# Optimization experiments

Hardware: AMD Instinct MI355X
Metric: run time of the kernel (lower is better)

Reference implementation:

```python
import jax, jax.numpy as jnp
import numpy as np
from jax import lax

N, C, RC, H, W = 2, 256, 32, 64, 64  # RC = C // 8


def conv1x1(x, w, b):
    # x: [n,c,h,w], w: [o,c], b: [o]
    return jnp.einsum('nchw,oc->nohw', x, w) + b[None, :, None, None]


def conv3x3(x, w, b):
    # x: [n,c,h,w], w: [o,i,3,3]
    y = lax.conv_general_dilated(x, w, window_strides=(1, 1), padding='SAME',
                                 dimension_numbers=('NCHW', 'OIHW', 'NCHW'))
    return y + b[None, :, None, None]


def setup_inputs() -> dict:
    key = jax.random.key(0)
    ks = jax.random.split(key, 16)
    p = lambda k, s: jax.random.normal(k, s, dtype=jnp.float32) * 0.02
    z = lambda o: jnp.zeros((o,), jnp.float32)
    return {
        'rgb_feat': jax.random.normal(ks[0], (N, C, H, W), jnp.float32),
        'chm_feat': jax.random.normal(ks[1], (N, C, H, W), jnp.float32),
        'rgb_q_w': p(ks[2], (RC, C)), 'rgb_q_b': z(RC),
        'rgb_k_w': p(ks[3], (RC, C)), 'rgb_k_b': z(RC),
        'rgb_v_w': p(ks[4], (C, C)), 'rgb_v_b': z(C),
        'depth_q_w': p(ks[5], (RC, C)), 'depth_q_b': z(RC),
        'depth_k_w': p(ks[6], (RC, C)), 'depth_k_b': z(RC),
        'depth_v_w': p(ks[7], (C, C)), 'depth_v_b': z(C),
        'gate_w': p(ks[8], (C, 2 * C)), 'gate_b': z(C),
        'fus1_w': p(ks[9], (2 * C, 2 * C)), 'fus1_b': z(2 * C),
        'fus2_w': p(ks[10], (2 * C, 2 * C, 3, 3)), 'fus2_b': z(2 * C),
        'fus3_w': p(ks[11], (C, 2 * C)), 'fus3_b': z(C),
        'skip_w': p(ks[12], (C, 2 * C)), 'skip_b': z(C),
    }


def reference(rgb_feat, chm_feat,
              rgb_q_w, rgb_q_b, rgb_k_w, rgb_k_b, rgb_v_w, rgb_v_b,
              depth_q_w, depth_q_b, depth_k_w, depth_k_b, depth_v_w, depth_v_b,
              gate_w, gate_b, fus1_w, fus1_b, fus2_w, fus2_b,
              fus3_w, fus3_b, skip_w, skip_b):
    n, c, h, w = rgb_feat.shape
    hw = h * w
    flat = lambda t: t.reshape(n, t.shape[1], hw)

    rq = flat(conv1x1(rgb_feat, rgb_q_w, rgb_q_b))       # [n,rc,hw]
    rk = flat(conv1x1(rgb_feat, rgb_k_w, rgb_k_b))       # [n,rc,hw]
    rv = flat(conv1x1(rgb_feat, rgb_v_w, rgb_v_b))       # [n,c,hw]
    dq = flat(conv1x1(chm_feat, depth_q_w, depth_q_b))   # [n,rc,hw]
    dk = flat(conv1x1(chm_feat, depth_k_w, depth_k_b))   # [n,rc,hw]
    dv = flat(conv1x1(chm_feat, depth_v_w, depth_v_b))   # [n,c,hw]

    # rgb branch attended with depth-derived attention
    rgb_attn = jax.nn.softmax(jnp.einsum('nri,nrj->nij', dq, dk), axis=-1)  # [n,hw,hw]
    br = jnp.einsum('nci,nij->ncj', rv, rgb_attn).reshape(rgb_feat.shape) + rgb_feat

    # depth branch attended with rgb-derived attention
    depth_attn = jax.nn.softmax(jnp.einsum('nri,nrj->nij', rq, rk), axis=-1)
    bd = jnp.einsum('nci,nij->ncj', dv, depth_attn).reshape(chm_feat.shape) + chm_feat

    cat = jnp.concatenate([br, bd], axis=1)              # [n,2c,h,w]
    g = jax.nn.sigmoid(conv1x1(cat, gate_w, gate_b))     # [n,c,h,w]
    c_fused = br * g + bd * (1.0 - g)
    d_fused = br * bd
    f = jnp.concatenate([c_fused, d_fused], axis=1)      # [n,2c,h,w]

    y = jax.nn.relu(conv1x1(f, fus1_w, fus1_b))
    y = jax.nn.relu(conv3x3(y, fus2_w, fus2_b))
    y = conv1x1(y, fus3_w, fus3_b)
    fused = y + conv1x1(f, skip_w, skip_b)
    return fused
```

## Files before the change

### kernel.cpp

```cpp
#include <hip/hip_runtime.h>
#include <stdint.h>


typedef __bf16 bf16_t;
typedef __bf16 bf16x8 __attribute__((ext_vector_type(8)));
typedef float f32x4 __attribute__((ext_vector_type(4)));

#define HW 4096
#define NB 2

__device__ inline f32x4 mfma_bf16(bf16x8 a, bf16x8 b, f32x4 c) {
    return __builtin_amdgcn_mfma_f32_16x16x32_bf16(a, b, c, 0, 0, 0);
}

#define MAXJOB 12
struct CvtJobs {
    const float* src[MAXJOB];
    bf16_t* dst[MAXJOB];
    int vend[MAXJOB];
    int rowlen[MAXJOB];
    int rowstride[MAXJOB];
    int rowoff[MAXJOB];
};

__global__ __launch_bounds__(256) void convert_batch_k(CvtJobs J, int totalvec) {
    int gv = blockIdx.x * 256 + threadIdx.x;
    if (gv >= totalvec) return;
    int j = 0;
    while (gv >= J.vend[j]) j++;
    int vbase = (j == 0) ? 0 : J.vend[j - 1];
    int e = (gv - vbase) * 8;
    const float* s = J.src[j] + e;
    float4 f0 = *(const float4*)s;
    float4 f1 = *(const float4*)(s + 4);
    bf16x8 o;
    o[0] = (bf16_t)f0.x; o[1] = (bf16_t)f0.y; o[2] = (bf16_t)f0.z; o[3] = (bf16_t)f0.w;
    o[4] = (bf16_t)f1.x; o[5] = (bf16_t)f1.y; o[6] = (bf16_t)f1.z; o[7] = (bf16_t)f1.w;
    int di = e;
    if (J.rowlen[j])
        di = (e / J.rowlen[j]) * J.rowstride[j] + J.rowoff[j] + (e % J.rowlen[j]);
    *(bf16x8*)(J.dst[j] + di) = o;
}

__global__ __launch_bounds__(256) void pack_bias_k(const float* qr, const float* kr,
                                                   const float* qd, const float* kd,
                                                   const float* sb, const float* fb,
                                                   float* BQK_R, float* BQK_D, float* BSUM) {
    int t = threadIdx.x;
    if (t < 32) {
        BQK_R[t] = qr[t]; BQK_R[32 + t] = kr[t];
        BQK_D[t] = qd[t]; BQK_D[32 + t] = kd[t];
    }
    BSUM[t] = sb[t] + fb[t];
}

__global__ __launch_bounds__(256) void reorder_fus2_k(const float* __restrict__ src,
                                                      bf16_t* __restrict__ dst) {
    int idx = blockIdx.x * 256 + threadIdx.x;
    if (idx >= 512 * 4608) return;
    int o = idx / 4608;
    int t = idx % 4608;
    int t9 = t / 512;
    int c  = t % 512;
    dst[idx] = (bf16_t)src[(size_t)o * 4608 + c * 9 + t9];
}

template <int EPI, bool OUT_BF16>
__global__ __launch_bounds__(256) void gemm_k(const bf16_t* __restrict__ A,
                                              const bf16_t* __restrict__ A2,
                                              const bf16_t* __restrict__ B,
                                              const float* __restrict__ bias,
                                              const float* __restrict__ bias2,
                                              void* __restrict__ outp,
                                              const void* __restrict__ aux,
                                              int M, int K, size_t strideB, size_t strideO) {
    __shared__ bf16_t Bt[64][72];
    const int t = threadIdx.x;
    const int mb = blockIdx.x, jb = blockIdx.y, n = blockIdx.z;
    const int w = t >> 6, lane = t & 63, quad = lane >> 4, l16 = lane & 15;

    const bf16_t* Au = (n >= 2) ? A2 : A;
    const float* biasu = (n >= 2) ? bias2 : bias;

    const bf16_t* Bb = B + (size_t)n * strideB + jb * 64;
    const int srow = t >> 2;
    const int scol = (t & 3) << 4;

    f32x4 zero = {0.f, 0.f, 0.f, 0.f};
    f32x4 acc[4] = {zero, zero, zero, zero};

    const bf16_t* Arow = Au + (size_t)(mb * 64 + w * 16 + l16) * K + quad * 8;

    for (int k0 = 0; k0 < K; k0 += 64) {
        const bf16_t* src = Bb + (size_t)(k0 + srow) * HW + scol;
        bf16x8 v0 = *(const bf16x8*)src;
        bf16x8 v1 = *(const bf16x8*)(src + 8);
        __syncthreads();
#pragma unroll
        for (int e = 0; e < 8; e++) Bt[scol + e][srow] = v0[e];
#pragma unroll
        for (int e = 0; e < 8; e++) Bt[scol + 8 + e][srow] = v1[e];
        __syncthreads();

        bf16x8 a0 = *(const bf16x8*)(Arow + k0);
        bf16x8 a1 = *(const bf16x8*)(Arow + k0 + 32);
#pragma unroll
        for (int ns = 0; ns < 4; ns++) {
            bf16x8 b0 = *(const bf16x8*)&Bt[ns * 16 + l16][quad * 8];
            bf16x8 b1 = *(const bf16x8*)&Bt[ns * 16 + l16][32 + quad * 8];
            acc[ns] = mfma_bf16(a0, b0, acc[ns]);
            acc[ns] = mfma_bf16(a1, b1, acc[ns]);
        }
    }

    if (EPI == 6) {
#pragma unroll
        for (int ns = 0; ns < 4; ns++) {
            int col = jb * 64 + ns * 16 + l16;
            union { bf16_t h[4]; unsigned long long u; } pk;
#pragma unroll
            for (int rr = 0; rr < 4; rr++) {
                int m = w * 16 + quad * 4 + rr;
                pk.h[rr] = (bf16_t)(acc[ns][rr] + biasu[m]);
            }
            *(unsigned long long*)((bf16_t*)outp +
                ((size_t)n * HW + col) * 64 + w * 16 + quad * 4) = pk.u;
        }
    } else if (EPI == 7) {
        const int m_base = mb * 64 + w * 16 + quad * 4;
#pragma unroll
        for (int ns = 0; ns < 4; ns++) {
            int col = jb * 64 + ns * 16 + l16;
            union { bf16_t h[4]; unsigned long long u; } pk;
#pragma unroll
            for (int rr = 0; rr < 4; rr++) {
                float v = acc[ns][rr] + biasu[m_base + rr];
                pk.h[rr] = (bf16_t)(v > 0.f ? v : 0.f);
            }
            *(unsigned long long*)((bf16_t*)outp +
                ((size_t)n * HW + col) * 512 + m_base) = pk.u;
        }
    } else if (EPI == 5) {
        const bf16_t* catp = (const bf16_t*)aux;
        bf16_t* f = (bf16_t*)outp;
#pragma unroll
        for (int ns = 0; ns < 4; ns++) {
#pragma unroll
            for (int rr = 0; rr < 4; rr++) {
                int m = mb * 64 + w * 16 + quad * 4 + rr;
                int col = jb * 64 + ns * 16 + l16;
                float v = acc[ns][rr] + biasu[m];
                float g = 1.f / (1.f + __expf(-v));
                size_t base = (size_t)n * 512 * HW + (size_t)m * HW + col;
                float br = (float)catp[base];
                float bd = (float)catp[base + (size_t)256 * HW];
                size_t ob = (size_t)n * 1024 * HW + (size_t)m * HW + col;
                f[ob] = (bf16_t)(br * g + bd * (1.f - g));
                f[ob + (size_t)256 * HW] = (bf16_t)(br * bd);
            }
        }
    } else {
#pragma unroll
        for (int ns = 0; ns < 4; ns++) {
#pragma unroll
            for (int rr = 0; rr < 4; rr++) {
                int m = mb * 64 + w * 16 + quad * 4 + rr;
                int col = jb * 64 + ns * 16 + l16;
                float v = acc[ns][rr] + biasu[m];
                if (EPI == 1) v = v > 0.f ? v : 0.f;
                size_t oi = (size_t)n * strideO + (size_t)m * HW + col;
                if (OUT_BF16) ((bf16_t*)outp)[oi] = (bf16_t)v;
                else ((float*)outp)[oi] = v;
            }
        }
    }
}

__global__ __launch_bounds__(256) void conv3_k(const bf16_t* __restrict__ A,
                                               const bf16_t* __restrict__ Y1n,
                                               const float* __restrict__ bias,
                                               bf16_t* __restrict__ outp,
                                               size_t strideN) {
    __shared__ bf16_t kTn[198][72];
    const int t = threadIdx.x;
    const int mb = blockIdx.x, y = blockIdx.y, n = blockIdx.z;
    const int w = t >> 6, lane = t & 63, quad = lane >> 4, l16 = lane & 15;

    f32x4 zero = {0.f, 0.f, 0.f, 0.f};
    f32x4 acc[2][4];
#pragma unroll
    for (int i = 0; i < 2; i++)
#pragma unroll
        for (int j = 0; j < 4; j++) acc[i][j] = zero;

    const bf16_t* Yb = Y1n + (size_t)n * HW * 512;

    const bf16_t* Arow0 = A + (size_t)(mb * 128 + w * 32 + l16) * 4608 + quad * 8;
    const bf16_t* Arow1 = Arow0 + (size_t)16 * 4608;

    int pxs[7], seg[7], gidx[7];
    bool ok[7], act[7];
#pragma unroll
    for (int i = 0; i < 7; i++) {
        int slot = t + i * 256;
        act[i] = slot < 1584;
        int ps = act[i] ? (slot >> 3) : 0;
        pxs[i] = ps;
        seg[i] = slot & 7;
        int r = ps / 66, xm = ps % 66;
        int yy = y + r - 1, xx = xm - 1;
        ok[i] = act[i] && ((unsigned)yy < 64u) && ((unsigned)xx < 64u);
        gidx[i] = ok[i] ? (yy * 64 + xx) : 0;
    }

    for (int c0 = 0; c0 < 512; c0 += 64) {
        bf16x8 vals[7];
#pragma unroll
        for (int i = 0; i < 7; i++) {
            bf16x8 v;
            if (ok[i]) {
                v = *(const bf16x8*)(Yb + (size_t)gidx[i] * 512 + c0 + seg[i] * 8);
            } else {
#pragma unroll
                for (int e = 0; e < 8; e++) v[e] = (bf16_t)0.f;
            }
            vals[i] = v;
        }
        __syncthreads();
#pragma unroll
        for (int i = 0; i < 7; i++)
            if (act[i]) *(bf16x8*)&kTn[pxs[i]][seg[i] * 8] = vals[i];
        __syncthreads();

#pragma unroll
        for (int t9 = 0; t9 < 9; t9++) {
            const int dy = t9 / 3, dx = t9 % 3;
            const bf16_t* ap0 = Arow0 + t9 * 512 + c0;
            const bf16_t* ap1 = Arow1 + t9 * 512 + c0;
            bf16x8 a00 = *(const bf16x8*)(ap0);
            bf16x8 a01 = *(const bf16x8*)(ap0 + 32);
            bf16x8 a10 = *(const bf16x8*)(ap1);
            bf16x8 a11 = *(const bf16x8*)(ap1 + 32);
#pragma unroll
            for (int ns = 0; ns < 4; ns++) {
                int p = dy * 66 + ns * 16 + l16 + dx;
                bf16x8 b0 = *(const bf16x8*)&kTn[p][quad * 8];
                bf16x8 b1 = *(const bf16x8*)&kTn[p][32 + quad * 8];
                acc[0][ns] = mfma_bf16(a00, b0, acc[0][ns]);
                acc[0][ns] = mfma_bf16(a01, b1, acc[0][ns]);
                acc[1][ns] = mfma_bf16(a10, b0, acc[1][ns]);
                acc[1][ns] = mfma_bf16(a11, b1, acc[1][ns]);
            }
        }
    }

#pragma unroll
    for (int ms = 0; ms < 2; ms++) {
#pragma unroll
        for (int ns = 0; ns < 4; ns++) {
#pragma unroll
            for (int rr = 0; rr < 4; rr++) {
                int m = mb * 128 + w * 32 + ms * 16 + quad * 4 + rr;
                int x = ns * 16 + l16;
                float v = acc[ms][ns][rr] + bias[m];
                v = v > 0.f ? v : 0.f;
                outp[(size_t)n * strideN + (size_t)m * HW + y * 64 + x] = (bf16_t)v;
            }
        }
    }
}

__global__ __launch_bounds__(256) void attn3_k(const bf16_t* __restrict__ QKT,
                                               const bf16_t* __restrict__ V,
                                               const float* __restrict__ rgb_feat,
                                               const float* __restrict__ chm_feat,
                                               bf16_t* __restrict__ CAT) {
    __shared__ bf16_t PT[2][64][72];
    __shared__ float Zp[4][64];
    const int t = threadIdx.x;
    const int lin = blockIdx.x;
    const int cb = lin & 1, z = (lin >> 1) & 3, jb = lin >> 3;
    const int w = t >> 6, lane = t & 63, quad = lane >> 4, l16 = lane & 15;
    const int qs = z ^ 2, n = z & 1;

    const bf16_t* Q = QKT + (size_t)qs * HW * 64;

    bf16x8 bS[4];
#pragma unroll
    for (int ns = 0; ns < 4; ns++)
        bS[ns] = *(const bf16x8*)(Q + (size_t)(jb * 64 + ns * 16 + l16) * 64 + 32 + quad * 8);

    f32x4 zero = {0.f, 0.f, 0.f, 0.f};
    f32x4 acc[2][4];
#pragma unroll
    for (int i = 0; i < 2; i++)
#pragma unroll
        for (int j = 0; j < 4; j++) acc[i][j] = zero;
    float zacc[4] = {0.f, 0.f, 0.f, 0.f};

    const bf16_t* Vr0 = V + ((size_t)z * 256 + cb * 128 + w * 16 + l16) * HW + quad * 8;
    const bf16_t* Vr1 = Vr0 + (size_t)64 * HW;

    for (int it = 0; it < 64; it++) {
        const int p = it & 1;
        bf16x8 aS = *(const bf16x8*)(Q + (size_t)(it * 64 + w * 16 + l16) * 64 + quad * 8);
        bf16x8 aV[2][2];
        aV[0][0] = *(const bf16x8*)(Vr0 + it * 64);
        aV[0][1] = *(const bf16x8*)(Vr0 + it * 64 + 32);
        aV[1][0] = *(const bf16x8*)(Vr1 + it * 64);
        aV[1][1] = *(const bf16x8*)(Vr1 + it * 64 + 32);

#pragma unroll
        for (int ns = 0; ns < 4; ns++) {
            f32x4 s = mfma_bf16(aS, bS[ns], zero);
            union { bf16_t h[4]; unsigned long long u; } pk;
            float zs = 0.f;
#pragma unroll
            for (int rr = 0; rr < 4; rr++) {
                pk.h[rr] = (bf16_t)__expf(s[rr]);
                zs += (float)pk.h[rr];
            }
            zacc[ns] += zs;
            *(unsigned long long*)&PT[p][ns * 16 + l16][w * 16 + quad * 4] = pk.u;
        }
        asm volatile("s_waitcnt lgkmcnt(0)" ::: "memory");
        __builtin_amdgcn_s_barrier();
        __builtin_amdgcn_sched_barrier(0);

        __builtin_amdgcn_s_setprio(1);
#pragma unroll
        for (int ns = 0; ns < 4; ns++) {
            bf16x8 b0 = *(const bf16x8*)&PT[p][ns * 16 + l16][quad * 8];
            bf16x8 b1 = *(const bf16x8*)&PT[p][ns * 16 + l16][32 + quad * 8];
#pragma unroll
            for (int ct = 0; ct < 2; ct++) {
                acc[ct][ns] = mfma_bf16(aV[ct][0], b0, acc[ct][ns]);
                acc[ct][ns] = mfma_bf16(aV[ct][1], b1, acc[ct][ns]);
            }
        }
        __builtin_amdgcn_s_setprio(0);
    }

#pragma unroll
    for (int ns = 0; ns < 4; ns++) {
        zacc[ns] += __shfl_xor(zacc[ns], 16, 64);
        zacc[ns] += __shfl_xor(zacc[ns], 32, 64);
    }
    if (lane < 16) {
#pragma unroll
        for (int ns = 0; ns < 4; ns++) Zp[w][ns * 16 + lane] = zacc[ns];
    }
    __syncthreads();
    float rz[4];
#pragma unroll
    for (int ns = 0; ns < 4; ns++) {
        float ssum = 0.f;
#pragma unroll
        for (int ww = 0; ww < 4; ww++) ssum += Zp[ww][ns * 16 + l16];
        rz[ns] = 1.f / ssum;
    }

    const float* feat = ((z < 2) ? rgb_feat : chm_feat) + (size_t)n * 256 * HW;
    bf16_t* outp = CAT + (size_t)n * 512 * HW + (size_t)(z < 2 ? 0 : 256) * HW;
#pragma unroll
    for (int ct = 0; ct < 2; ct++) {
#pragma unroll
        for (int ns = 0; ns < 4; ns++) {
#pragma unroll
            for (int rr = 0; rr < 4; rr++) {
                int c = cb * 128 + ct * 64 + w * 16 + quad * 4 + rr;
                int col = jb * 64 + ns * 16 + l16;
                float v = acc[ct][ns][rr] * rz[ns] + feat[(size_t)c * HW + col];
                outp[(size_t)c * HW + col] = (bf16_t)v;
            }
        }
    }
}

extern "C" void kernel_launch(void* const* d_in, const int* in_sizes, int n_in,
                              void* d_out, int out_size, void* d_ws, size_t ws_size,
                              hipStream_t stream) {
    (void)in_sizes; (void)n_in; (void)out_size; (void)ws_size;

    const float* rgb_feat  = (const float*)d_in[0];
    const float* chm_feat  = (const float*)d_in[1];
    const float* rgb_q_w   = (const float*)d_in[2];
    const float* rgb_q_b   = (const float*)d_in[3];
    const float* rgb_k_w   = (const float*)d_in[4];
    const float* rgb_k_b   = (const float*)d_in[5];
    const float* rgb_v_w   = (const float*)d_in[6];
    const float* rgb_v_b   = (const float*)d_in[7];
    const float* depth_q_w = (const float*)d_in[8];
    const float* depth_q_b = (const float*)d_in[9];
    const float* depth_k_w = (const float*)d_in[10];
    const float* depth_k_b = (const float*)d_in[11];
    const float* depth_v_w = (const float*)d_in[12];
    const float* depth_v_b = (const float*)d_in[13];
    const float* gate_w    = (const float*)d_in[14];
    const float* gate_b    = (const float*)d_in[15];
    const float* fus1_w    = (const float*)d_in[16];
    const float* fus1_b    = (const float*)d_in[17];
    const float* fus2_w    = (const float*)d_in[18];
    const float* fus2_b    = (const float*)d_in[19];
    const float* fus3_w    = (const float*)d_in[20];
    const float* fus3_b    = (const float*)d_in[21];
    const float* skip_w    = (const float*)d_in[22];
    const float* skip_b    = (const float*)d_in[23];

    char* ws = (char*)d_ws;
    size_t off = 0;
    auto alloc = [&](size_t bytes) -> char* {
        char* p = ws + off;
        off += (bytes + 255) & ~(size_t)255;
        return p;
    };

    bf16_t* WQK_R = (bf16_t*)alloc(64 * 256 * 2);
    bf16_t* WQK_D = (bf16_t*)alloc(64 * 256 * 2);
    bf16_t* WV_R  = (bf16_t*)alloc(256 * 256 * 2);
    bf16_t* WV_D  = (bf16_t*)alloc(256 * 256 * 2);
    bf16_t* WGATE = (bf16_t*)alloc(256 * 512 * 2);
    bf16_t* WFUS1 = (bf16_t*)alloc(512 * 512 * 2);
    bf16_t* WFUS2 = (bf16_t*)alloc(512 * 4608 * 2);
    bf16_t* WCAT  = (bf16_t*)alloc(256 * 1024 * 2);
    float*  BQK_R = (float*)alloc(64 * 4);
    float*  BQK_D = (float*)alloc(64 * 4);
    float*  BSUM  = (float*)alloc(256 * 4);
    bf16_t* XB    = (bf16_t*)alloc((size_t)4 * 256 * HW * 2);
    bf16_t* QKT   = (bf16_t*)alloc((size_t)4 * HW * 64 * 2);
    bf16_t* V4    = (bf16_t*)alloc((size_t)4 * 256 * HW * 2);
    bf16_t* CAT   = (bf16_t*)alloc((size_t)NB * 512 * HW * 2);
    bf16_t* FY    = (bf16_t*)alloc((size_t)NB * 1024 * HW * 2);
    bf16_t* Y1    = (bf16_t*)alloc((size_t)NB * HW * 512 * 2);

    bf16_t* XR = XB;
    bf16_t* XC = XB + (size_t)2 * 256 * HW;

    CvtJobs J;
    int cum = 0, nj = 0;
    auto addjob = [&](const float* s, bf16_t* d, int cnt, int rl, int rs, int ro) {
        J.src[nj] = s; J.dst[nj] = d; cum += cnt / 8; J.vend[nj] = cum;
        J.rowlen[nj] = rl; J.rowstride[nj] = rs; J.rowoff[nj] = ro; nj++;
    };
    addjob(rgb_feat, XR, NB * 256 * HW, 0, 0, 0);
    addjob(chm_feat, XC, NB * 256 * HW, 0, 0, 0);
    addjob(rgb_q_w, WQK_R, 32 * 256, 0, 0, 0);
    addjob(rgb_k_w, WQK_R + 32 * 256, 32 * 256, 0, 0, 0);
    addjob(depth_q_w, WQK_D, 32 * 256, 0, 0, 0);
    addjob(depth_k_w, WQK_D + 32 * 256, 32 * 256, 0, 0, 0);
    addjob(rgb_v_w, WV_R, 256 * 256, 0, 0, 0);
    addjob(depth_v_w, WV_D, 256 * 256, 0, 0, 0);
    addjob(gate_w, WGATE, 256 * 512, 0, 0, 0);
    addjob(fus1_w, WFUS1, 512 * 512, 0, 0, 0);
    addjob(skip_w, WCAT, 256 * 512, 512, 1024, 0);
    addjob(fus3_w, WCAT, 256 * 512, 512, 1024, 512);
    int totalvec = cum;
    convert_batch_k<<<dim3((totalvec + 255) / 256), 256, 0, stream>>>(J, totalvec);
    reorder_fus2_k<<<dim3(512 * 4608 / 256), 256, 0, stream>>>(fus2_w, WFUS2);
    pack_bias_k<<<dim3(1), 256, 0, stream>>>(rgb_q_b, rgb_k_b, depth_q_b, depth_k_b,
                                             skip_b, fus3_b, BQK_R, BQK_D, BSUM);

    gemm_k<6, true><<<dim3(1, 64, 4), 256, 0, stream>>>(
        WQK_R, WQK_D, XB, BQK_R, BQK_D, QKT, nullptr, 64, 256, (size_t)256 * HW, 0);

    gemm_k<0, true><<<dim3(4, 64, 4), 256, 0, stream>>>(
        WV_R, WV_D, XB, rgb_v_b, depth_v_b, V4, nullptr, 256, 256, (size_t)256 * HW, (size_t)256 * HW);

    attn3_k<<<dim3(512), 256, 0, stream>>>(QKT, V4, rgb_feat, chm_feat, CAT);

    gemm_k<5, true><<<dim3(4, 64, NB), 256, 0, stream>>>(
        WGATE, WGATE, CAT, gate_b, gate_b, FY, CAT, 256, 512, (size_t)512 * HW, 0);

    gemm_k<7, true><<<dim3(8, 64, NB), 256, 0, stream>>>(
        WFUS1, WFUS1, FY, fus1_b, fus1_b, Y1, nullptr, 512, 512, (size_t)1024 * HW, 0);

    conv3_k<<<dim3(4, 64, NB), 256, 0, stream>>>(WFUS2, Y1, fus2_b,
                                                 FY + (size_t)512 * HW, (size_t)1024 * HW);

    gemm_k<0, false><<<dim3(4, 64, NB), 256, 0, stream>>>(
        WCAT, WCAT, FY, BSUM, BSUM, d_out, nullptr, 256, 1024, (size_t)1024 * HW, (size_t)256 * HW);
}
```

Baseline: 342.7 us.

## Prefetch next attention tile operands and use exp2 with log2e-prescaled queries

The attention loop is unrolled by two with ping-pong register sets, so the next iteration's Q and V fragments are loaded from global memory while the current tile's exp and PV MFMAs run. This hides global load latency behind compute. The projection epilogue now scales the query half of the QK output by log2(e), which lets the kernel call the native exp2 instruction instead of __expf. The cost is higher register pressure, plus one redundant wrapped load on the final iteration.

Measured after the change: 344.3 us. Within noise of the previous version (+0.5%).

```diff
diff --git a/kernel.cpp b/kernel.cpp
--- a/kernel.cpp
+++ b/kernel.cpp
@@ -114,6 +114,7 @@
     }
 
     if (EPI == 6) {
+        const float scl = (w < 2) ? 1.44269504f : 1.0f;
 #pragma unroll
         for (int ns = 0; ns < 4; ns++) {
             int col = jb * 64 + ns * 16 + l16;
@@ -121,7 +122,7 @@
 #pragma unroll
             for (int rr = 0; rr < 4; rr++) {
                 int m = w * 16 + quad * 4 + rr;
-                pk.h[rr] = (bf16_t)(acc[ns][rr] + biasu[m]);
+                pk.h[rr] = (bf16_t)((acc[ns][rr] + biasu[m]) * scl);
             }
             *(unsigned long long*)((bf16_t*)outp +
                 ((size_t)n * HW + col) * 64 + w * 16 + quad * 4) = pk.u;
@@ -269,6 +270,43 @@
         }
     }
 }
+
+#define ASTEP(P, ASC, AVC, ASN, AVN, ITN)                                      \
+    {                                                                          \
+        _Pragma("unroll")                                                      \
+        for (int ns = 0; ns < 4; ns++) {                                       \
+            f32x4 s = mfma_bf16(ASC, bS[ns], zero);                            \
+            union { bf16_t h[4]; unsigned long long u; } pk;                   \
+            float zs = 0.f;                                                    \
+            _Pragma("unroll")                                                  \
+            for (int rr = 0; rr < 4; rr++) {                                   \
+                pk.h[rr] = (bf16_t)__builtin_amdgcn_exp2f(s[rr]);              \
+                zs += (float)pk.h[rr];                                         \
+            }                                                                  \
+            zacc[ns] += zs;                                                    \
+            *(unsigned long long*)&PT[P][ns * 16 + l16][w * 16 + quad * 4] = pk.u; \
+        }                                                                      \
+        ASN = *(const bf16x8*)(Qa + (size_t)((ITN) & 63) * (64 * 64));         \
+        AVN[0][0] = *(const bf16x8*)(Vr0 + ((ITN) & 63) * 64);                 \
+        AVN[0][1] = *(const bf16x8*)(Vr0 + ((ITN) & 63) * 64 + 32);            \
+        AVN[1][0] = *(const bf16x8*)(Vr1 + ((ITN) & 63) * 64);                 \
+        AVN[1][1] = *(const bf16x8*)(Vr1 + ((ITN) & 63) * 64 + 32);            \
+        asm volatile("s_waitcnt lgkmcnt(0)" ::: "memory");                     \
+        __builtin_amdgcn_s_barrier();                                          \
+        __builtin_amdgcn_sched_barrier(0);                                     \
+        __builtin_amdgcn_s_setprio(1);                                         \
+        _Pragma("unroll")                                                      \
+        for (int ns = 0; ns < 4; ns++) {                                       \
+            bf16x8 b0 = *(const bf16x8*)&PT[P][ns * 16 + l16][quad * 8];       \
+            bf16x8 b1 = *(const bf16x8*)&PT[P][ns * 16 + l16][32 + quad * 8];  \
+            _Pragma("unroll")                                                  \
+            for (int ct = 0; ct < 2; ct++) {                                   \
+                acc[ct][ns] = mfma_bf16(AVC[ct][0], b0, acc[ct][ns]);          \
+                acc[ct][ns] = mfma_bf16(AVC[ct][1], b1, acc[ct][ns]);          \
+            }                                                                  \
+        }                                                                      \
+        __builtin_amdgcn_s_setprio(0);                                         \
+    }
 
 __global__ __launch_bounds__(256) void attn3_k(const bf16_t* __restrict__ QKT,
                                                const bf16_t* __restrict__ V,
@@ -300,45 +338,18 @@
 
     const bf16_t* Vr0 = V + ((size_t)z * 256 + cb * 128 + w * 16 + l16) * HW + quad * 8;
     const bf16_t* Vr1 = Vr0 + (size_t)64 * HW;
-
-    for (int it = 0; it < 64; it++) {
-        const int p = it & 1;
-        bf16x8 aS = *(const bf16x8*)(Q + (size_t)(it * 64 + w * 16 + l16) * 64 + quad * 8);
-        bf16x8 aV[2][2];
-        aV[0][0] = *(const bf16x8*)(Vr0 + it * 64);
-        aV[0][1] = *(const bf16x8*)(Vr0 + it * 64 + 32);
-        aV[1][0] = *(const bf16x8*)(Vr1 + it * 64);
-        aV[1][1] = *(const bf16x8*)(Vr1 + it * 64 + 32);
-
-#pragma unroll
-        for (int ns = 0; ns < 4; ns++) {
-            f32x4 s = mfma_bf16(aS, bS[ns], zero);
-            union { bf16_t h[4]; unsigned long long u; } pk;
-            float zs = 0.f;
-#pragma unroll
-            for (int rr = 0; rr < 4; rr++) {
-                pk.h[rr] = (bf16_t)__expf(s[rr]);
-                zs += (float)pk.h[rr];
-            }
-            zacc[ns] += zs;
-            *(unsigned long long*)&PT[p][ns * 16 + l16][w * 16 + quad * 4] = pk.u;
-        }
-        asm volatile("s_waitcnt lgkmcnt(0)" ::: "memory");
-        __builtin_amdgcn_s_barrier();
-        __builtin_amdgcn_sched_barrier(0);
-
-        __builtin_amdgcn_s_setprio(1);
-#pragma unroll
-        for (int ns = 0; ns < 4; ns++) {
-            bf16x8 b0 = *(const bf16x8*)&PT[p][ns * 16 + l16][quad * 8];
-            bf16x8 b1 = *(const bf16x8*)&PT[p][ns * 16 + l16][32 + quad * 8];
-#pragma unroll
-            for (int ct = 0; ct < 2; ct++) {
-                acc[ct][ns] = mfma_bf16(aV[ct][0], b0, acc[ct][ns]);
-                acc[ct][ns] = mfma_bf16(aV[ct][1], b1, acc[ct][ns]);
-            }
-        }
-        __builtin_amdgcn_s_setprio(0);
+    const bf16_t* Qa = Q + (size_t)(w * 16 + l16) * 64 + quad * 8;
+
+    bf16x8 aSa, aSb, aVa[2][2], aVb[2][2];
+    aSa = *(const bf16x8*)Qa;
+    aVa[0][0] = *(const bf16x8*)(Vr0);
+    aVa[0][1] = *(const bf16x8*)(Vr0 + 32);
+    aVa[1][0] = *(const bf16x8*)(Vr1);
+    aVa[1][1] = *(const bf16x8*)(Vr1 + 32);
+
+    for (int ii = 0; ii < 32; ii++) {
+        ASTEP(0, aSa, aVa, aSb, aVb, 2 * ii + 1);
+        ASTEP(1, aSb, aVb, aSa, aVa, 2 * ii + 2);
     }
 
 #pragma unroll
```
